# Optimization experiments

Measured on AMD Instinct MI355X. Metric: run time of the kernel, lower is better.

The kernel has to match this reference:

```python
import jax, jax.numpy as jnp
import numpy as np

DIM = 1024
QK_DIM = 1024
V_DIM = 1024
HEADS = 16


def setup_inputs() -> dict:
    key = jax.random.key(0)
    k1, k2, k3, k4 = jax.random.split(key, 4)
    x = jax.random.normal(k1, (4, 2048, DIM), dtype=jnp.float32)
    context = jax.random.normal(k2, (4, 2048, DIM), dtype=jnp.float32)
    # Linear weights stored as (in, out) so y = x @ W; scaled like torch default init
    Wq = jax.random.normal(k3, (DIM, QK_DIM), dtype=jnp.float32) / np.sqrt(DIM)
    Wkv = jax.random.normal(k4, (DIM, QK_DIM + V_DIM), dtype=jnp.float32) / np.sqrt(DIM)
    return {"x": x, "context": context, "Wq": Wq, "Wkv": Wkv}


def reference(x, context, Wq, Wkv):
    b, n, _ = x.shape
    j = context.shape[1]
    h = HEADS
    dqk = QK_DIM // h
    dv = V_DIM // h
    q = x @ Wq                                  # [b, n, qk_dim]
    kv = context @ Wkv                          # [b, j, qk_dim + v_dim]
    k, v = kv[..., :QK_DIM], kv[..., QK_DIM:]
    # split heads: b n (h d) -> b h n d
    q = q.reshape(b, n, h, dqk).transpose(0, 2, 1, 3)
    k = k.reshape(b, j, h, dqk).transpose(0, 2, 1, 3)
    v = v.reshape(b, j, h, dv).transpose(0, 2, 1, 3)
    scale = dqk ** -0.5
    scores = jnp.einsum('bhid,bhjd->bhij', q * scale, k)  # [b, h, n, j]
    weights = jax.nn.softmax(scores, axis=-1)
    attn = jnp.einsum('bhij,bhjd->bhid', weights, v)       # [b, h, n, dv]
    out = attn.transpose(0, 2, 1, 3).reshape(b, n, h * dv)
    return out
```

## Files before the change

### kernel.cpp

```cpp
#include <hip/hip_runtime.h>
#include <hip/hip_bf16.h>

using bf16 = __hip_bfloat16;
typedef __bf16 bf16x8 __attribute__((ext_vector_type(8)));
typedef float f32x4 __attribute__((ext_vector_type(4)));

#define DEV static __device__ __forceinline__

DEV void gld_lds16(const bf16* g, bf16* l) {
  __builtin_amdgcn_global_load_lds((__attribute__((address_space(1))) void*)g,
                                   (__attribute__((address_space(3))) void*)l,
                                   16, 0, 0);
}

template<int NCHUNK>
DEV void stage_tile(const bf16* g, int gs, bf16* lds) {
  const int tid = threadIdx.x;
  const int w = tid >> 6, lane = tid & 63;
#pragma unroll
  for (int i = 0; i < NCHUNK / 256; ++i) {
    const int pb = i * 256 + w * 64;
    const int p  = pb + lane;
    const int r  = p >> 3;
    const int c  = (p & 7) ^ (r & 7);
    gld_lds16(g + r * gs + c * 8, lds + pb * 8);
  }
}

DEV bf16x8 frag(const bf16* lds, int row, int cchunk) {
  const int p = row * 8 + (cchunk ^ (row & 7));
  return *(const bf16x8*)(lds + p * 8);
}

__global__ void cvt_bf16_2(const float4* __restrict__ in0, ushort4* __restrict__ out0,
                           const float4* __restrict__ in1, ushort4* __restrict__ out1,
                           int n4) {
  int i = blockIdx.x * 256 + threadIdx.x;
  const int stride = gridDim.x * 256;
  for (; i < n4; i += stride) {
    float4 a = in0[i];
    float4 b = in1[i];
    union { ushort4 u; bf16 h[4]; } oa, ob;
    oa.h[0] = __float2bfloat16(a.x); oa.h[1] = __float2bfloat16(a.y);
    oa.h[2] = __float2bfloat16(a.z); oa.h[3] = __float2bfloat16(a.w);
    ob.h[0] = __float2bfloat16(b.x); ob.h[1] = __float2bfloat16(b.y);
    ob.h[2] = __float2bfloat16(b.z); ob.h[3] = __float2bfloat16(b.w);
    out0[i] = oa.u;
    out1[i] = ob.u;
  }
}

__global__ void transpose_w2(const float* __restrict__ wq, bf16* __restrict__ wqt,
                             const float* __restrict__ wkv, bf16* __restrict__ wkvt) {
  __shared__ float t[32][33];
  const float* in; bf16* out; int N; float scale;
  int bx = blockIdx.x;
  if (bx < 32) { in = wq;  out = wqt;  N = 1024; scale = 0.18033688011112042f; }
  else         { in = wkv; out = wkvt; N = 2048; scale = 1.0f; bx -= 32; }
  const int k0 = blockIdx.y * 32, n0 = bx * 32;
  const int tx = threadIdx.x, ty = threadIdx.y;
#pragma unroll
  for (int s = 0; s < 4; ++s)
    t[ty + 8 * s][tx] = in[(size_t)(k0 + ty + 8 * s) * N + n0 + tx];
  __syncthreads();
#pragma unroll
  for (int s = 0; s < 4; ++s)
    out[(size_t)(n0 + ty + 8 * s) * 1024 + k0 + tx] =
        __float2bfloat16(t[tx][ty + 8 * s] * scale);
}

__global__ __launch_bounds__(256, 3)
void gemm_all(const bf16* __restrict__ xb, const bf16* __restrict__ cb,
              const bf16* __restrict__ wqt, const bf16* __restrict__ wkvt,
              bf16* __restrict__ qb, bf16* __restrict__ kb, bf16* __restrict__ vtb) {
  __shared__ alignas(16) bf16 As[128 * 64];
  __shared__ alignas(16) bf16 Bs[128 * 64];
  const int id = blockIdx.x;
  const bool isq = id < 512;
  const bf16* A; const bf16* Bt; bf16* outN; int m0, n0;
  if (isq) {
    A = xb; Bt = wqt; outN = qb;
    n0 = (id & 7) * 128;  m0 = (id >> 3) * 128;
  } else {
    const int id2 = id - 512;
    A = cb; Bt = wkvt; outN = kb;
    n0 = (id2 & 15) * 128; m0 = (id2 >> 4) * 128;
  }
  const int tid = threadIdx.x, lane = tid & 63, w = tid >> 6;
  const int q4 = lane >> 4, cc = lane & 15;
  const int wr = (w >> 1) * 64, wc = (w & 1) * 64;

  f32x4 acc[4][4] = {};
  for (int k0 = 0; k0 < 1024; k0 += 64) {
    stage_tile<1024>(A + (size_t)m0 * 1024 + k0, 1024, As);
    stage_tile<1024>(Bt + (size_t)n0 * 1024 + k0, 1024, Bs);
    __syncthreads();
#pragma unroll
    for (int ks = 0; ks < 2; ++ks) {
      bf16x8 af[4], bfr[4];
#pragma unroll
      for (int i = 0; i < 4; ++i) af[i] = frag(As, wr + i * 16 + cc, ks * 4 + q4);
#pragma unroll
      for (int j = 0; j < 4; ++j) bfr[j] = frag(Bs, wc + j * 16 + cc, ks * 4 + q4);
#pragma unroll
      for (int i = 0; i < 4; ++i)
#pragma unroll
        for (int j = 0; j < 4; ++j)
          acc[i][j] = __builtin_amdgcn_mfma_f32_16x16x32_bf16(af[i], bfr[j],
                                                              acc[i][j], 0, 0, 0);
    }
    __syncthreads();
  }
#pragma unroll
  for (int i = 0; i < 4; ++i) {
    const int gm = m0 + wr + i * 16 + q4 * 4;
    const int b = gm >> 11, ntok0 = gm & 2047;
#pragma unroll
    for (int j = 0; j < 4; ++j) {
      const int gc = n0 + wc + j * 16 + cc;
#pragma unroll
      for (int r = 0; r < 4; ++r) {
        const bf16 hv = __float2bfloat16(acc[i][j][r]);
        const int n = ntok0 + r;
        if (isq || gc < 1024) {
          const int h = (gc >> 6) & 15, d = gc & 63;
          outN[(size_t)(b * 16 + h) * 131072 + (size_t)n * 64 + d] = hv;
        } else {
          const int gc2 = gc - 1024, h = gc2 >> 6, d = gc2 & 63;
          vtb[(size_t)(b * 16 + h) * 131072 + (size_t)d * 2048 + n] = hv;
        }
      }
    }
  }
}

__global__ __launch_bounds__(256, 4)
void attn(const bf16* __restrict__ Q, const bf16* __restrict__ Km,
          const bf16* __restrict__ VT, float* __restrict__ out) {
  __shared__ alignas(16) char smem[18432 + 8192 + 8192];
  bf16* Qs  = (bf16*)smem;
  bf16* Ps  = (bf16*)smem;
  bf16* Ks  = (bf16*)(smem + 18432);
  bf16* VTs = (bf16*)(smem + 26624);
  const int tid = threadIdx.x, lane = tid & 63, w = tid >> 6;
  const int q4 = lane >> 4, cc = lane & 15;
  const int bh = blockIdx.y;
  const int it0 = blockIdx.x * 128;
  const bf16* Qg = Q + (size_t)bh * 131072 + (size_t)it0 * 64;
  const bf16* Kg = Km + (size_t)bh * 131072;
  const bf16* Vg = VT + (size_t)bh * 131072;

  stage_tile<1024>(Qg, 64, Qs);
  __syncthreads();
  bf16x8 qf[2][2];
#pragma unroll
  for (int it = 0; it < 2; ++it)
#pragma unroll
    for (int ks = 0; ks < 2; ++ks)
      qf[it][ks] = frag(Qs, w * 32 + it * 16 + cc, ks * 4 + q4);

  f32x4 o_acc[2][4] = {};
  float lsum[2][4] = {};
  bf16* Pw = Ps + w * (32 * 72);

  for (int j0 = 0; j0 < 2048; j0 += 64) {
    stage_tile<512>(Kg + (size_t)j0 * 64, 64, Ks);
    stage_tile<512>(Vg + j0, 2048, VTs);
    __syncthreads();
    f32x4 s[2][4] = {};
#pragma unroll
    for (int ks = 0; ks < 2; ++ks) {
      bf16x8 kb[4];
#pragma unroll
      for (int jt = 0; jt < 4; ++jt) kb[jt] = frag(Ks, jt * 16 + cc, ks * 4 + q4);
#pragma unroll
      for (int it = 0; it < 2; ++it)
#pragma unroll
        for (int jt = 0; jt < 4; ++jt)
          s[it][jt] = __builtin_amdgcn_mfma_f32_16x16x32_bf16(qf[it][ks], kb[jt],
                                                              s[it][jt], 0, 0, 0);
    }
#pragma unroll
    for (int it = 0; it < 2; ++it)
#pragma unroll
      for (int jt = 0; jt < 4; ++jt)
#pragma unroll
        for (int r = 0; r < 4; ++r) {
          const float p = __builtin_amdgcn_exp2f(s[it][jt][r]);
          lsum[it][r] += p;
          Pw[(it * 16 + q4 * 4 + r) * 72 + jt * 16 + cc] = __float2bfloat16(p);
        }
    asm volatile("s_waitcnt lgkmcnt(0)" ::: "memory");
#pragma unroll
    for (int ks = 0; ks < 2; ++ks) {
      bf16x8 pa[2], vb[4];
#pragma unroll
      for (int it = 0; it < 2; ++it)
        pa[it] = *(const bf16x8*)(Pw + (it * 16 + cc) * 72 + ks * 32 + q4 * 8);
#pragma unroll
      for (int dt = 0; dt < 4; ++dt) vb[dt] = frag(VTs, dt * 16 + cc, ks * 4 + q4);
#pragma unroll
      for (int it = 0; it < 2; ++it)
#pragma unroll
        for (int dt = 0; dt < 4; ++dt)
          o_acc[it][dt] = __builtin_amdgcn_mfma_f32_16x16x32_bf16(pa[it], vb[dt],
                                                                  o_acc[it][dt], 0, 0, 0);
    }
    __syncthreads();
  }
#pragma unroll
  for (int it = 0; it < 2; ++it)
#pragma unroll
    for (int r = 0; r < 4; ++r) {
      float v = lsum[it][r];
      v += __shfl_xor(v, 1); v += __shfl_xor(v, 2);
      v += __shfl_xor(v, 4); v += __shfl_xor(v, 8);
      lsum[it][r] = 1.0f / v;
    }
  const int b = bh >> 4, h = bh & 15;
#pragma unroll
  for (int it = 0; it < 2; ++it)
#pragma unroll
    for (int r = 0; r < 4; ++r) {
      const int n = it0 + w * 32 + it * 16 + q4 * 4 + r;
      const float inv = lsum[it][r];
      const size_t base = ((size_t)b * 2048 + n) * 1024 + h * 64;
#pragma unroll
      for (int dt = 0; dt < 4; ++dt)
        out[base + dt * 16 + cc] = o_acc[it][dt][r] * inv;
    }
}

extern "C" void kernel_launch(void* const* d_in, const int* in_sizes, int n_in,
                              void* d_out, int out_size, void* d_ws, size_t ws_size,
                              hipStream_t stream) {
  const float* x   = (const float*)d_in[0];
  const float* ctx = (const float*)d_in[1];
  const float* Wq  = (const float*)d_in[2];
  const float* Wkv = (const float*)d_in[3];
  float* out = (float*)d_out;
  char* ws = (char*)d_ws;
  bf16* xb   = (bf16*)(ws);
  bf16* cb   = (bf16*)(ws + 16777216);
  bf16* wqt  = (bf16*)(ws + 33554432);
  bf16* wkvt = (bf16*)(ws + 35651584);
  bf16* qb   = (bf16*)(ws + 39845888);
  bf16* kb   = (bf16*)(ws + 56623104);
  bf16* vtb  = (bf16*)(ws + 73400320);

  cvt_bf16_2<<<2048, 256, 0, stream>>>((const float4*)x, (ushort4*)xb,
                                       (const float4*)ctx, (ushort4*)cb, 8388608 / 4);
  transpose_w2<<<dim3(96, 32), dim3(32, 8), 0, stream>>>(Wq, wqt, Wkv, wkvt);
  gemm_all<<<1536, 256, 0, stream>>>(xb, cb, wqt, wkvt, qb, kb, vtb);
  attn<<<dim3(16, 64), 256, 0, stream>>>(qb, kb, vtb, out);
}
```

Baseline: 300.0 us.

## Keep softmax probabilities in registers via transposed MFMA and vectorize stores

The attention kernel now computes S^T = K·Q^T with permuted K rows, so each lane's exp'd scores can be packed directly into the B operand of the P·V MFMA. This removes the LDS round trip for P and shrinks shared memory to the K and V tiles. The GEMM swaps operand order so Q/K/V outputs are written as packed 4-element bf16 vectors, and the attention output is written as float4. The two prep kernels are merged into one launch, and Q fragments are loaded straight from global memory. The risks are the fragment-layout correctness and possibly higher register pressure.

New measurement: 372.6 us. +24.2%, slower.

```diff
diff --git a/kernel.cpp b/kernel.cpp
--- a/kernel.cpp
+++ b/kernel.cpp
@@ -32,33 +32,45 @@
   return *(const bf16x8*)(lds + p * 8);
 }
 
-__global__ void cvt_bf16_2(const float4* __restrict__ in0, ushort4* __restrict__ out0,
-                           const float4* __restrict__ in1, ushort4* __restrict__ out1,
-                           int n4) {
-  int i = blockIdx.x * 256 + threadIdx.x;
-  const int stride = gridDim.x * 256;
-  for (; i < n4; i += stride) {
-    float4 a = in0[i];
-    float4 b = in1[i];
-    union { ushort4 u; bf16 h[4]; } oa, ob;
-    oa.h[0] = __float2bfloat16(a.x); oa.h[1] = __float2bfloat16(a.y);
-    oa.h[2] = __float2bfloat16(a.z); oa.h[3] = __float2bfloat16(a.w);
-    ob.h[0] = __float2bfloat16(b.x); ob.h[1] = __float2bfloat16(b.y);
-    ob.h[2] = __float2bfloat16(b.z); ob.h[3] = __float2bfloat16(b.w);
-    out0[i] = oa.u;
-    out1[i] = ob.u;
-  }
-}
-
-__global__ void transpose_w2(const float* __restrict__ wq, bf16* __restrict__ wqt,
-                             const float* __restrict__ wkv, bf16* __restrict__ wkvt) {
+DEV unsigned pk2(float a, float b) {
+  union { bf16 h; unsigned short s; } lo, hi;
+  lo.h = __float2bfloat16(a); hi.h = __float2bfloat16(b);
+  return (unsigned)lo.s | ((unsigned)hi.s << 16);
+}
+
+union FragU { int i[4]; bf16x8 v; };
+
+__global__ void prep(const float4* __restrict__ x, ushort4* __restrict__ xb,
+                     const float4* __restrict__ ctx, ushort4* __restrict__ cb,
+                     const float* __restrict__ wq, bf16* __restrict__ wqt,
+                     const float* __restrict__ wkv, bf16* __restrict__ wkvt) {
   __shared__ float t[32][33];
+  const int tid = threadIdx.x;
+  if (blockIdx.x < 2048) {
+    int i = blockIdx.x * 256 + tid;
+    const int stride = 2048 * 256;
+#pragma unroll
+    for (int s = 0; s < 4; ++s, i += stride) {
+      float4 a = x[i];
+      float4 b = ctx[i];
+      union { ushort4 u; bf16 h[4]; } oa, ob;
+      oa.h[0] = __float2bfloat16(a.x); oa.h[1] = __float2bfloat16(a.y);
+      oa.h[2] = __float2bfloat16(a.z); oa.h[3] = __float2bfloat16(a.w);
+      ob.h[0] = __float2bfloat16(b.x); ob.h[1] = __float2bfloat16(b.y);
+      ob.h[2] = __float2bfloat16(b.z); ob.h[3] = __float2bfloat16(b.w);
+      xb[i] = oa.u;
+      cb[i] = ob.u;
+    }
+    return;
+  }
+  const int tb = blockIdx.x - 2048;
+  int bx = tb % 96;
+  const int by = tb / 96;
   const float* in; bf16* out; int N; float scale;
-  int bx = blockIdx.x;
   if (bx < 32) { in = wq;  out = wqt;  N = 1024; scale = 0.18033688011112042f; }
   else         { in = wkv; out = wkvt; N = 2048; scale = 1.0f; bx -= 32; }
-  const int k0 = blockIdx.y * 32, n0 = bx * 32;
-  const int tx = threadIdx.x, ty = threadIdx.y;
+  const int k0 = by * 32, n0 = bx * 32;
+  const int tx = tid & 31, ty = tid >> 5;
 #pragma unroll
   for (int s = 0; s < 4; ++s)
     t[ty + 8 * s][tx] = in[(size_t)(k0 + ty + 8 * s) * N + n0 + tx];
@@ -86,6 +98,7 @@
     A = cb; Bt = wkvt; outN = kb;
     n0 = (id2 & 15) * 128; m0 = (id2 >> 4) * 128;
   }
+  const bool swapped = isq || (n0 < 1024);
   const int tid = threadIdx.x, lane = tid & 63, w = tid >> 6;
   const int q4 = lane >> 4, cc = lane & 15;
   const int wr = (w >> 1) * 64, wc = (w & 1) * 64;
@@ -102,33 +115,53 @@
       for (int i = 0; i < 4; ++i) af[i] = frag(As, wr + i * 16 + cc, ks * 4 + q4);
 #pragma unroll
       for (int j = 0; j < 4; ++j) bfr[j] = frag(Bs, wc + j * 16 + cc, ks * 4 + q4);
-#pragma unroll
-      for (int i = 0; i < 4; ++i)
-#pragma unroll
-        for (int j = 0; j < 4; ++j)
-          acc[i][j] = __builtin_amdgcn_mfma_f32_16x16x32_bf16(af[i], bfr[j],
-                                                              acc[i][j], 0, 0, 0);
-    }
-    __syncthreads();
-  }
-#pragma unroll
-  for (int i = 0; i < 4; ++i) {
-    const int gm = m0 + wr + i * 16 + q4 * 4;
-    const int b = gm >> 11, ntok0 = gm & 2047;
-#pragma unroll
-    for (int j = 0; j < 4; ++j) {
-      const int gc = n0 + wc + j * 16 + cc;
-#pragma unroll
-      for (int r = 0; r < 4; ++r) {
-        const bf16 hv = __float2bfloat16(acc[i][j][r]);
-        const int n = ntok0 + r;
-        if (isq || gc < 1024) {
-          const int h = (gc >> 6) & 15, d = gc & 63;
-          outN[(size_t)(b * 16 + h) * 131072 + (size_t)n * 64 + d] = hv;
-        } else {
-          const int gc2 = gc - 1024, h = gc2 >> 6, d = gc2 & 63;
-          vtb[(size_t)(b * 16 + h) * 131072 + (size_t)d * 2048 + n] = hv;
-        }
+      if (swapped) {
+#pragma unroll
+        for (int i = 0; i < 4; ++i)
+#pragma unroll
+          for (int j = 0; j < 4; ++j)
+            acc[i][j] = __builtin_amdgcn_mfma_f32_16x16x32_bf16(bfr[j], af[i],
+                                                                acc[i][j], 0, 0, 0);
+      } else {
+#pragma unroll
+        for (int i = 0; i < 4; ++i)
+#pragma unroll
+          for (int j = 0; j < 4; ++j)
+            acc[i][j] = __builtin_amdgcn_mfma_f32_16x16x32_bf16(af[i], bfr[j],
+                                                                acc[i][j], 0, 0, 0);
+      }
+    }
+    __syncthreads();
+  }
+  const int b = m0 >> 11;
+  if (swapped) {
+#pragma unroll
+    for (int i = 0; i < 4; ++i) {
+      const int token = m0 + wr + i * 16 + cc;
+      const int n = token & 2047;
+#pragma unroll
+      for (int j = 0; j < 4; ++j) {
+        const int f0 = n0 + wc + j * 16 + q4 * 4;
+        const int h = f0 >> 6, d0 = f0 & 63;
+        uint2 pv;
+        pv.x = pk2(acc[i][j][0], acc[i][j][1]);
+        pv.y = pk2(acc[i][j][2], acc[i][j][3]);
+        *(uint2*)(outN + ((size_t)(b * 16 + h)) * 131072 + (size_t)n * 64 + d0) = pv;
+      }
+    }
+  } else {
+#pragma unroll
+    for (int i = 0; i < 4; ++i) {
+      const int t0 = m0 + wr + i * 16 + q4 * 4;
+      const int nn = t0 & 2047;
+#pragma unroll
+      for (int j = 0; j < 4; ++j) {
+        const int gc2 = (n0 - 1024) + wc + j * 16 + cc;
+        const int h = gc2 >> 6, din = gc2 & 63;
+        uint2 pv;
+        pv.x = pk2(acc[i][j][0], acc[i][j][1]);
+        pv.y = pk2(acc[i][j][2], acc[i][j][3]);
+        *(uint2*)(vtb + ((size_t)(b * 16 + h)) * 131072 + (size_t)din * 2048 + nn) = pv;
       }
     }
   }
@@ -137,11 +170,8 @@
 __global__ __launch_bounds__(256, 4)
 void attn(const bf16* __restrict__ Q, const bf16* __restrict__ Km,
           const bf16* __restrict__ VT, float* __restrict__ out) {
-  __shared__ alignas(16) char smem[18432 + 8192 + 8192];
-  bf16* Qs  = (bf16*)smem;
-  bf16* Ps  = (bf16*)smem;
-  bf16* Ks  = (bf16*)(smem + 18432);
-  bf16* VTs = (bf16*)(smem + 26624);
+  __shared__ alignas(16) bf16 Ks[64 * 64];
+  __shared__ alignas(16) bf16 VTs[64 * 64];
   const int tid = threadIdx.x, lane = tid & 63, w = tid >> 6;
   const int q4 = lane >> 4, cc = lane & 15;
   const int bh = blockIdx.y;
@@ -150,85 +180,93 @@
   const bf16* Kg = Km + (size_t)bh * 131072;
   const bf16* Vg = VT + (size_t)bh * 131072;
 
-  stage_tile<1024>(Qg, 64, Qs);
-  __syncthreads();
   bf16x8 qf[2][2];
 #pragma unroll
   for (int it = 0; it < 2; ++it)
 #pragma unroll
     for (int ks = 0; ks < 2; ++ks)
-      qf[it][ks] = frag(Qs, w * 32 + it * 16 + cc, ks * 4 + q4);
-
-  f32x4 o_acc[2][4] = {};
-  float lsum[2][4] = {};
-  bf16* Pw = Ps + w * (32 * 72);
+      qf[it][ks] = *(const bf16x8*)(Qg + (size_t)(w * 32 + it * 16 + cc) * 64 +
+                                    ks * 32 + q4 * 8);
+
+  const int krow_lo = (cc >> 2) * 8 + (cc & 3);
+
+  f32x4 o_t[4][2] = {};
+  float lsum[2] = {};
 
   for (int j0 = 0; j0 < 2048; j0 += 64) {
     stage_tile<512>(Kg + (size_t)j0 * 64, 64, Ks);
     stage_tile<512>(Vg + j0, 2048, VTs);
     __syncthreads();
-    f32x4 s[2][4] = {};
+    f32x4 st[4][2] = {};
 #pragma unroll
     for (int ks = 0; ks < 2; ++ks) {
-      bf16x8 kb[4];
-#pragma unroll
-      for (int jt = 0; jt < 4; ++jt) kb[jt] = frag(Ks, jt * 16 + cc, ks * 4 + q4);
-#pragma unroll
-      for (int it = 0; it < 2; ++it)
-#pragma unroll
-        for (int jt = 0; jt < 4; ++jt)
-          s[it][jt] = __builtin_amdgcn_mfma_f32_16x16x32_bf16(qf[it][ks], kb[jt],
-                                                              s[it][jt], 0, 0, 0);
-    }
-#pragma unroll
-    for (int it = 0; it < 2; ++it)
+      bf16x8 kf[4];
 #pragma unroll
       for (int jt = 0; jt < 4; ++jt)
-#pragma unroll
-        for (int r = 0; r < 4; ++r) {
-          const float p = __builtin_amdgcn_exp2f(s[it][jt][r]);
-          lsum[it][r] += p;
-          Pw[(it * 16 + q4 * 4 + r) * 72 + jt * 16 + cc] = __float2bfloat16(p);
-        }
-    asm volatile("s_waitcnt lgkmcnt(0)" ::: "memory");
+        kf[jt] = frag(Ks, (jt >> 1) * 32 + (jt & 1) * 4 + krow_lo, ks * 4 + q4);
+#pragma unroll
+      for (int jt = 0; jt < 4; ++jt)
+#pragma unroll
+        for (int it = 0; it < 2; ++it)
+          st[jt][it] = __builtin_amdgcn_mfma_f32_16x16x32_bf16(kf[jt], qf[it][ks],
+                                                               st[jt][it], 0, 0, 0);
+    }
+    int pk[4][2][2];
+#pragma unroll
+    for (int jt = 0; jt < 4; ++jt)
+#pragma unroll
+      for (int it = 0; it < 2; ++it) {
+        float e0 = __builtin_amdgcn_exp2f(st[jt][it][0]);
+        float e1 = __builtin_amdgcn_exp2f(st[jt][it][1]);
+        float e2 = __builtin_amdgcn_exp2f(st[jt][it][2]);
+        float e3 = __builtin_amdgcn_exp2f(st[jt][it][3]);
+        lsum[it] += (e0 + e1) + (e2 + e3);
+        pk[jt][it][0] = (int)pk2(e0, e1);
+        pk[jt][it][1] = (int)pk2(e2, e3);
+      }
 #pragma unroll
     for (int ks = 0; ks < 2; ++ks) {
-      bf16x8 pa[2], vb[4];
-#pragma unroll
-      for (int it = 0; it < 2; ++it)
-        pa[it] = *(const bf16x8*)(Pw + (it * 16 + cc) * 72 + ks * 32 + q4 * 8);
-#pragma unroll
-      for (int dt = 0; dt < 4; ++dt) vb[dt] = frag(VTs, dt * 16 + cc, ks * 4 + q4);
-#pragma unroll
-      for (int it = 0; it < 2; ++it)
+      bf16x8 vf[4];
+#pragma unroll
+      for (int dt = 0; dt < 4; ++dt) vf[dt] = frag(VTs, dt * 16 + cc, ks * 4 + q4);
+#pragma unroll
+      for (int it = 0; it < 2; ++it) {
+        FragU fu;
+        fu.i[0] = pk[2 * ks][it][0];
+        fu.i[1] = pk[2 * ks][it][1];
+        fu.i[2] = pk[2 * ks + 1][it][0];
+        fu.i[3] = pk[2 * ks + 1][it][1];
 #pragma unroll
         for (int dt = 0; dt < 4; ++dt)
-          o_acc[it][dt] = __builtin_amdgcn_mfma_f32_16x16x32_bf16(pa[it], vb[dt],
-                                                                  o_acc[it][dt], 0, 0, 0);
-    }
-    __syncthreads();
-  }
-#pragma unroll
-  for (int it = 0; it < 2; ++it)
-#pragma unroll
-    for (int r = 0; r < 4; ++r) {
-      float v = lsum[it][r];
-      v += __shfl_xor(v, 1); v += __shfl_xor(v, 2);
-      v += __shfl_xor(v, 4); v += __shfl_xor(v, 8);
-      lsum[it][r] = 1.0f / v;
-    }
+          o_t[dt][it] = __builtin_amdgcn_mfma_f32_16x16x32_bf16(vf[dt], fu.v,
+                                                                o_t[dt][it], 0, 0, 0);
+      }
+    }
+    __syncthreads();
+  }
+  float inv[2];
+#pragma unroll
+  for (int it = 0; it < 2; ++it) {
+    float v = lsum[it];
+    v += __shfl_xor(v, 16);
+    v += __shfl_xor(v, 32);
+    inv[it] = 1.0f / v;
+  }
   const int b = bh >> 4, h = bh & 15;
 #pragma unroll
-  for (int it = 0; it < 2; ++it)
-#pragma unroll
-    for (int r = 0; r < 4; ++r) {
-      const int n = it0 + w * 32 + it * 16 + q4 * 4 + r;
-      const float inv = lsum[it][r];
-      const size_t base = ((size_t)b * 2048 + n) * 1024 + h * 64;
-#pragma unroll
-      for (int dt = 0; dt < 4; ++dt)
-        out[base + dt * 16 + cc] = o_acc[it][dt][r] * inv;
-    }
+  for (int it = 0; it < 2; ++it) {
+    const int n = it0 + w * 32 + it * 16 + cc;
+    const size_t base = ((size_t)b * 2048 + n) * 1024 + h * 64 + q4 * 4;
+#pragma unroll
+    for (int dt = 0; dt < 4; ++dt) {
+      float4 val;
+      val.x = o_t[dt][it][0] * inv[it];
+      val.y = o_t[dt][it][1] * inv[it];
+      val.z = o_t[dt][it][2] * inv[it];
+      val.w = o_t[dt][it][3] * inv[it];
+      *(float4*)(out + base + dt * 16) = val;
+    }
+  }
 }
 
 extern "C" void kernel_launch(void* const* d_in, const int* in_sizes, int n_in,
@@ -248,9 +286,9 @@
   bf16* kb   = (bf16*)(ws + 56623104);
   bf16* vtb  = (bf16*)(ws + 73400320);
 
-  cvt_bf16_2<<<2048, 256, 0, stream>>>((const float4*)x, (ushort4*)xb,
-                                       (const float4*)ctx, (ushort4*)cb, 8388608 / 4);
-  transpose_w2<<<dim3(96, 32), dim3(32, 8), 0, stream>>>(Wq, wqt, Wkv, wkvt);
+  prep<<<5120, 256, 0, stream>>>((const float4*)x, (ushort4*)xb,
+                                 (const float4*)ctx, (ushort4*)cb,
+                                 Wq, wqt, Wkv, wkvt);
   gemm_all<<<1536, 256, 0, stream>>>(xb, cb, wqt, wkvt, qb, kb, vtb);
   attn<<<dim3(16, 64), 256, 0, stream>>>(qb, kb, vtb, out);
 }
```
